# Performance work log

Measured on AMD Instinct MI355X. Metric: run time of the kernel, lower is better.

Reference implementation:

```python
import jax, jax.numpy as jnp
import numpy as np

S, B, H = 1024, 4, 1024
NH, NC = 16, 4            # num_attention_heads, num_combined_heads
HPH = H // NH             # 64
NF = NH // NC             # num_FFN = 4
FFM = 8                   # combined_FFN_multiple
DIN = NC * HPH            # 256, grouped FFN input dim
DHID = FFM * DIN          # 2048, dense_in output dim
DH2 = DHID // 2           # 1024, GLU half / dense_out input dim
EPS = 1e-6
NORM_FACTOR = 1.0 / float(np.sqrt(HPH))


def _ln(x, g, b):
    m = x.mean(-1, keepdims=True)
    v = ((x - m) ** 2).mean(-1, keepdims=True)
    return (x - m) * jax.lax.rsqrt(v + EPS) * g + b


def setup_inputs() -> dict:
    key = jax.random.key(0)
    ks = jax.random.split(key, 10)
    p = lambda k, shape: jax.random.normal(k, shape, jnp.float32) * 0.02
    return {
        "hidden_states": jax.random.normal(ks[0], (S, B, H), jnp.float32),
        "g1": jnp.ones((H,), jnp.float32), "b1": jnp.zeros((H,), jnp.float32),
        "g2": jnp.ones((HPH,), jnp.float32), "b2": jnp.zeros((HPH,), jnp.float32),
        "Wq": p(ks[1], (H, H)), "bq": jnp.zeros((H,), jnp.float32),
        "Wk": p(ks[2], (H, H)), "bk": jnp.zeros((H,), jnp.float32),
        "Wv": p(ks[3], (H, H)), "bv": jnp.zeros((H,), jnp.float32),
        "W_in": p(ks[4], (NF, DIN, DHID)), "b_in": jnp.zeros((NF, DHID), jnp.float32),
        "W_out": p(ks[5], (NF, DH2, DIN)), "b_out": jnp.zeros((NF, DIN), jnp.float32),
        "Wd": p(ks[6], (H, H)), "bd": jnp.zeros((H,), jnp.float32),
    }


def reference(hidden_states, g1, b1, g2, b2, Wq, bq, Wk, bk, Wv, bv,
              W_in, b_in, W_out, b_out, Wd, bd):
    # hidden_states: [S, B, H]
    x = _ln(hidden_states, g1, b1)                       # norm1

    def heads(t):  # [S,B,H] -> [B*NH, S, HPH] (matches view + transpose in torch)
        return jnp.transpose(t.reshape(S, B * NH, HPH), (1, 0, 2))

    q = heads(x @ Wq + bq)
    k = heads(x @ Wk + bk)
    v = heads(x @ Wv + bv)

    # subtraction_gaussian_kernel: pairwise squared euclidean distance
    qk = jnp.einsum('nsd,ntd->nst', q, k)                # [B*NH, S, S]
    q2 = jnp.sum(q * q, axis=-1)
    k2 = jnp.sum(k * k, axis=-1)
    dist = q2[:, :, None] + k2[None if False else slice(None), None, :][0] if False else q2[:, :, None] + k2[:, None, :] - 2.0 * qk
    matmul_result = dist * (-0.5 * NORM_FACTOR)          # scores <= 0

    # Exp sequence op: elementwise exp (softmax replacement, no normalization)
    probs = jnp.exp(matmul_result)

    ctx = jnp.einsum('nst,ntd->nsd', probs, v)           # [B*NH, S, HPH]
    ctx = jnp.transpose(ctx, (1, 0, 2)).reshape(S, B, H)
    ctx = x + ctx                                        # residual with norm1 output (as in source)

    ctx = _ln(ctx.reshape(S, B, NH, HPH), g2, b2)        # per-head norm2

    # grouped FFN over contiguous head subsets (vectorized over the NF groups)
    cg = ctx.reshape(S, B, NF, DIN)
    h = jnp.einsum('sbgi,gio->sbgo', cg, W_in) + b_in    # [S,B,NF,DHID]
    xh, yh = jnp.split(h, 2, axis=-1)
    h = xh * jax.nn.relu(yh)                             # GLU-style x * relu(y)
    og = jnp.einsum('sbgi,gio->sbgo', h, W_out) + b_out  # [S,B,NF,DIN]

    out = og.reshape(S, B, H) @ Wd + bd                  # attention_dense
    return out, matmul_result
```

## Files before the change

kernel.cpp:

```cpp
#include <hip/hip_runtime.h>


typedef __attribute__((ext_vector_type(8))) short short8;
typedef __attribute__((ext_vector_type(4))) float f32x4;

__device__ __forceinline__ unsigned short f2bf(float f) {
  union { float f; unsigned u; } x; x.f = f;
  unsigned r = x.u + 0x7FFFu + ((x.u >> 16) & 1u);
  return (unsigned short)(r >> 16);
}
__device__ __forceinline__ float bf2f(unsigned short u) {
  union { float f; unsigned u; } x; x.u = ((unsigned)u) << 16;
  return x.f;
}
__device__ __forceinline__ void gload16(const unsigned short* g, unsigned short* l) {
  __builtin_amdgcn_global_load_lds(
      (const __attribute__((address_space(1))) unsigned int*)g,
      (__attribute__((address_space(3))) unsigned int*)l, 16, 0, 0);
}

__global__ __launch_bounds__(256) void ln1_kernel(
    const float* __restrict__ x, const float* __restrict__ g,
    const float* __restrict__ b, float* __restrict__ y,
    unsigned short* __restrict__ ybf)
{
  const long base = (long)blockIdx.x * 1024;
  const int c = threadIdx.x * 4;
  float4 v = *(const float4*)(x + base + c);
  float s = v.x + v.y + v.z + v.w;
  float ss = v.x*v.x + v.y*v.y + v.z*v.z + v.w*v.w;
  #pragma unroll
  for (int off = 32; off > 0; off >>= 1) {
    s  += __shfl_xor(s, off);
    ss += __shfl_xor(ss, off);
  }
  __shared__ float sw[4], ssw[4];
  const int wave = threadIdx.x >> 6;
  if ((threadIdx.x & 63) == 0) { sw[wave] = s; ssw[wave] = ss; }
  __syncthreads();
  s  = sw[0] + sw[1] + sw[2] + sw[3];
  ss = ssw[0] + ssw[1] + ssw[2] + ssw[3];
  const float mean = s * (1.0f/1024.0f);
  const float var  = ss * (1.0f/1024.0f) - mean*mean;
  const float rs   = rsqrtf(var + 1e-6f);
  const float4 gv = *(const float4*)(g + c);
  const float4 bv = *(const float4*)(b + c);
  float4 o;
  o.x = (v.x - mean) * rs * gv.x + bv.x;
  o.y = (v.y - mean) * rs * gv.y + bv.y;
  o.z = (v.z - mean) * rs * gv.z + bv.z;
  o.w = (v.w - mean) * rs * gv.w + bv.w;
  *(float4*)(y + base + c) = o;
  ushort4 ob;
  ob.x = f2bf(o.x); ob.y = f2bf(o.y); ob.z = f2bf(o.z); ob.w = f2bf(o.w);
  *(ushort4*)(ybf + base + c) = ob;
}

__global__ __launch_bounds__(256) void transpose_w_kernel(
    const float* __restrict__ W, int K, int N, long wgs,
    unsigned short* __restrict__ WT, long wtgs)
{
  __shared__ float T[32][33];
  const float* Wg = W + (long)blockIdx.z * wgs;
  unsigned short* WTg = WT + (long)blockIdx.z * wtgs;
  const int n0 = blockIdx.x * 32, k0 = blockIdx.y * 32;
  const int t = threadIdx.x;
  const int r = t >> 3, c4 = (t & 7) * 4;
  float4 v = *(const float4*)(Wg + (long)(k0 + r) * N + n0 + c4);
  T[r][c4+0] = v.x; T[r][c4+1] = v.y; T[r][c4+2] = v.z; T[r][c4+3] = v.w;
  __syncthreads();
  ushort4 o;
  o.x = f2bf(T[c4+0][r]); o.y = f2bf(T[c4+1][r]);
  o.z = f2bf(T[c4+2][r]); o.w = f2bf(T[c4+3][r]);
  *(ushort4*)(WTg + (long)(n0 + r) * K + k0 + c4) = o;
}

__global__ __launch_bounds__(256) void transpose_qkvd_kernel(
    const float* __restrict__ Wq, const float* __restrict__ Wk,
    const float* __restrict__ Wv, const float* __restrict__ Wd,
    unsigned short* __restrict__ wqkvT, unsigned short* __restrict__ wdT)
{
  const int z = blockIdx.z;
  const float* W = (z == 0) ? Wq : (z == 1) ? Wk : (z == 2) ? Wv : Wd;
  unsigned short* WT = (z == 3) ? wdT : wqkvT + (long)z * 1048576;
  __shared__ float T[32][33];
  const int n0 = blockIdx.x * 32, k0 = blockIdx.y * 32;
  const int t = threadIdx.x;
  const int r = t >> 3, c4 = (t & 7) * 4;
  float4 v = *(const float4*)(W + (long)(k0 + r) * 1024 + n0 + c4);
  T[r][c4+0] = v.x; T[r][c4+1] = v.y; T[r][c4+2] = v.z; T[r][c4+3] = v.w;
  __syncthreads();
  ushort4 o;
  o.x = f2bf(T[c4+0][r]); o.y = f2bf(T[c4+1][r]);
  o.z = f2bf(T[c4+2][r]); o.w = f2bf(T[c4+3][r]);
  *(ushort4*)(WT + (long)(n0 + r) * 1024 + k0 + c4) = o;
}

__global__ __launch_bounds__(256) void packb_kernel(
    const float* __restrict__ bq, const float* __restrict__ bk,
    const float* __restrict__ bv, float* __restrict__ qb)
{
  const int i = blockIdx.x * 256 + threadIdx.x;
  qb[i] = (i < 1024) ? bq[i] : ((i < 2048) ? bk[i - 1024] : bv[i - 2048]);
}

__global__ __launch_bounds__(256) void mfma_gemm_kernel(
    const unsigned short* __restrict__ A, int lda, long agoff,
    const unsigned short* __restrict__ BT, long bgoff, int K,
    const float* __restrict__ bias, int biasoff,
    unsigned short* __restrict__ Cbf, float* __restrict__ Cf,
    int ldc, int cgoff)
{
  const int g = blockIdx.z;
  const unsigned short* Ag = A + (long)g * agoff;
  const unsigned short* Bg = BT + (long)g * bgoff;
  const float* biasg = bias + (long)g * biasoff;
  const int row0 = blockIdx.y * 128, col0 = blockIdx.x * 128;
  __shared__ __align__(16) unsigned short As[128 * 32];
  __shared__ __align__(16) unsigned short Bs[128 * 32];
  const int tid = threadIdx.x;
  const int w = tid >> 6, l = tid & 63;
  const int ms = (w & 1) << 6, ns = (w >> 1) << 6;
  const int fr = l & 15, fg = l >> 4;
  const int lr = l >> 2;
  const int sslot = (((l & 3) ^ (lr & 3)) << 3);
  const int arow = row0 + (w << 4) + lr;
  const int brow = col0 + (w << 4) + lr;
  const int rsw = fr & 3;
  f32x4 acc[4][4];
  #pragma unroll
  for (int i = 0; i < 4; ++i)
    #pragma unroll
    for (int j = 0; j < 4; ++j) acc[i][j] = (f32x4)0.0f;

  for (int k0 = 0; k0 < K; k0 += 32) {
    gload16(Ag + (long)arow * lda + k0 + sslot,        &As[(w << 4) * 32]);
    gload16(Ag + (long)(arow + 64) * lda + k0 + sslot, &As[(64 + (w << 4)) * 32]);
    gload16(Bg + (long)brow * K + k0 + sslot,          &Bs[(w << 4) * 32]);
    gload16(Bg + (long)(brow + 64) * K + k0 + sslot,   &Bs[(64 + (w << 4)) * 32]);
    __syncthreads();
    short8 af[4], bfr[4];
    #pragma unroll
    for (int i = 0; i < 4; ++i)
      af[i] = *(const short8*)&As[(ms + i*16 + fr) * 32 + ((fg ^ rsw) << 3)];
    #pragma unroll
    for (int j = 0; j < 4; ++j)
      bfr[j] = *(const short8*)&Bs[(ns + j*16 + fr) * 32 + ((fg ^ rsw) << 3)];
    #pragma unroll
    for (int i = 0; i < 4; ++i)
      #pragma unroll
      for (int j = 0; j < 4; ++j)
        acc[i][j] = __builtin_amdgcn_mfma_f32_16x16x32_bf16(af[i], bfr[j], acc[i][j], 0, 0, 0);
    __syncthreads();
  }

  float bj[4];
  #pragma unroll
  for (int j = 0; j < 4; ++j) bj[j] = biasg[col0 + ns + j*16 + fr];
  #pragma unroll
  for (int i = 0; i < 4; ++i)
    #pragma unroll
    for (int r = 0; r < 4; ++r) {
      const long row = row0 + ms + i*16 + (fg << 2) + r;
      const long cbase = row * ldc + (long)g * cgoff + col0 + ns;
      #pragma unroll
      for (int j = 0; j < 4; ++j) {
        const float v = acc[i][j][r] + bj[j];
        if (Cbf) Cbf[cbase + j*16 + fr] = f2bf(v);
        else     __builtin_nontemporal_store(v, &Cf[cbase + j*16 + fr]);
      }
    }
}

__global__ __launch_bounds__(256) void mfma_glu_kernel(
    const unsigned short* __restrict__ A,
    const unsigned short* __restrict__ WT,
    const float* __restrict__ bin,
    unsigned short* __restrict__ H2)
{
  const int g = blockIdx.z;
  const unsigned short* Ag = A + g * 256;
  const unsigned short* Wg = WT + (long)g * 2048 * 256;
  const float* bg = bin + g * 2048;
  const int row0 = blockIdx.y * 128, col0 = blockIdx.x * 64;
  __shared__ __align__(16) unsigned short As[128 * 32];
  __shared__ __align__(16) unsigned short Bxs[64 * 32];
  __shared__ __align__(16) unsigned short Bys[64 * 32];
  const int tid = threadIdx.x;
  const int w = tid >> 6, l = tid & 63;
  const int ms = (w & 1) << 6, ns = (w >> 1) << 5;
  const int fr = l & 15, fg = l >> 4;
  const int lr = l >> 2;
  const int sslot = (((l & 3) ^ (lr & 3)) << 3);
  const int arow = row0 + (w << 4) + lr;
  const int brow = col0 + (w << 4) + lr;
  const int rsw = fr & 3;
  f32x4 ax[4][2], ay[4][2];
  #pragma unroll
  for (int i = 0; i < 4; ++i)
    #pragma unroll
    for (int j = 0; j < 2; ++j) { ax[i][j] = (f32x4)0.0f; ay[i][j] = (f32x4)0.0f; }

  for (int k0 = 0; k0 < 256; k0 += 32) {
    gload16(Ag + (long)arow * 1024 + k0 + sslot,        &As[(w << 4) * 32]);
    gload16(Ag + (long)(arow + 64) * 1024 + k0 + sslot, &As[(64 + (w << 4)) * 32]);
    gload16(Wg + (long)brow * 256 + k0 + sslot,         &Bxs[(w << 4) * 32]);
    gload16(Wg + (long)(1024 + brow) * 256 + k0 + sslot,&Bys[(w << 4) * 32]);
    __syncthreads();
    short8 af[4], bx[2], by[2];
    #pragma unroll
    for (int i = 0; i < 4; ++i)
      af[i] = *(const short8*)&As[(ms + i*16 + fr) * 32 + ((fg ^ rsw) << 3)];
    #pragma unroll
    for (int j = 0; j < 2; ++j) {
      bx[j] = *(const short8*)&Bxs[(ns + j*16 + fr) * 32 + ((fg ^ rsw) << 3)];
      by[j] = *(const short8*)&Bys[(ns + j*16 + fr) * 32 + ((fg ^ rsw) << 3)];
    }
    #pragma unroll
    for (int i = 0; i < 4; ++i)
      #pragma unroll
      for (int j = 0; j < 2; ++j) {
        ax[i][j] = __builtin_amdgcn_mfma_f32_16x16x32_bf16(af[i], bx[j], ax[i][j], 0, 0, 0);
        ay[i][j] = __builtin_amdgcn_mfma_f32_16x16x32_bf16(af[i], by[j], ay[i][j], 0, 0, 0);
      }
    __syncthreads();
  }

  float bxb[2], byb[2];
  #pragma unroll
  for (int j = 0; j < 2; ++j) {
    bxb[j] = bg[col0 + ns + j*16 + fr];
    byb[j] = bg[1024 + col0 + ns + j*16 + fr];
  }
  #pragma unroll
  for (int i = 0; i < 4; ++i)
    #pragma unroll
    for (int r = 0; r < 4; ++r) {
      const long row = row0 + ms + i*16 + (fg << 2) + r;
      #pragma unroll
      for (int j = 0; j < 2; ++j) {
        const float xh = ax[i][j][r] + bxb[j];
        const float yh = ay[i][j][r] + byb[j];
        H2[row * 4096 + g * 1024 + col0 + ns + j*16 + fr] = f2bf(xh * fmaxf(yh, 0.0f));
      }
    }
}

__global__ __launch_bounds__(256) void sumsq_kernel(
    const unsigned short* __restrict__ qkv,
    float* __restrict__ q2g, float* __restrict__ k2g)
{
  const int sb = blockIdx.x;
  const int s = sb >> 2, b = sb & 3;
  const int h = threadIdx.x >> 4, e = threadIdx.x & 15;
  const long base = (long)sb * 3072 + h * 64 + e * 4;
  ushort4 qv = *(const ushort4*)(qkv + base);
  ushort4 kv = *(const ushort4*)(qkv + base + 1024);
  float sq = 0.f, sk = 0.f, f;
  f = bf2f(qv.x); sq = fmaf(f,f,sq); f = bf2f(qv.y); sq = fmaf(f,f,sq);
  f = bf2f(qv.z); sq = fmaf(f,f,sq); f = bf2f(qv.w); sq = fmaf(f,f,sq);
  f = bf2f(kv.x); sk = fmaf(f,f,sk); f = bf2f(kv.y); sk = fmaf(f,f,sk);
  f = bf2f(kv.z); sk = fmaf(f,f,sk); f = bf2f(kv.w); sk = fmaf(f,f,sk);
  #pragma unroll
  for (int off = 1; off < 16; off <<= 1) { sq += __shfl_xor(sq, off); sk += __shfl_xor(sk, off); }
  if (e == 0) {
    q2g[(b * 16 + h) * 1024 + s] = sq;
    k2g[(b * 16 + h) * 1024 + s] = sk;
  }
}

__global__ __launch_bounds__(256) void vtrans_kernel(
    const unsigned short* __restrict__ qkv, unsigned short* __restrict__ vt)
{
  __shared__ unsigned short T[64][72];
  const int n = blockIdx.y, s0 = blockIdx.x * 64;
  const int b = n >> 4, hoff = (n & 15) * 64;
  const int tid = threadIdx.x;
  #pragma unroll
  for (int p = 0; p < 2; ++p) {
    const int r = (tid >> 3) + p * 32, c = (tid & 7) << 3;
    *(short8*)&T[r][c] = *(const short8*)(qkv + ((long)((s0 + r) * 4 + b)) * 3072 + 2048 + hoff + c);
  }
  __syncthreads();
  #pragma unroll
  for (int p = 0; p < 2; ++p) {
    const int d = (tid >> 3) + p * 32, sc = (tid & 7) << 3;
    short8 o;
    #pragma unroll
    for (int j = 0; j < 8; ++j) o[j] = (short)T[sc + j][d];
    *(short8*)(vt + ((long)n * 64 + d) * 1024 + s0 + sc) = o;
  }
}

__global__ __launch_bounds__(256) void attn_kernel(
    const unsigned short* __restrict__ qkv, const unsigned short* __restrict__ vt,
    const float* __restrict__ q2g, const float* __restrict__ k2g,
    float* __restrict__ ctx, float* __restrict__ scores)
{
  const int n = blockIdx.y;
  const int s0 = blockIdx.x * 64;
  const int b = n >> 4, hoff = (n & 15) * 64;
  __shared__ __align__(16) unsigned short Qs[64][72];
  __shared__ __align__(16) unsigned short Ks[64 * 64];
  __shared__ __align__(16) unsigned short VTl[64 * 64];
  __shared__ __align__(16) unsigned short Ps[64][72];
  __shared__ float q2s[64];
  const int tid = threadIdx.x, w = tid >> 6, l = tid & 63;
  const int fr = l & 15, fg = l >> 4;
  const int lr8 = l >> 3, ls8 = l & 7;
  const int sslot = ((ls8 ^ lr8) << 3);
  const int rsw = fr & 7;

  #pragma unroll
  for (int p = 0; p < 2; ++p) {
    const int r = (tid >> 3) + p * 32, c = (tid & 7) << 3;
    *(short8*)&Qs[r][c] = *(const short8*)(qkv + ((long)((s0 + r) * 4 + b)) * 3072 + hoff + c);
  }
  if (tid < 64) q2s[tid] = q2g[n * 1024 + s0 + tid];

  f32x4 o[4];
  #pragma unroll
  for (int i = 0; i < 4; ++i) o[i] = (f32x4)0.0f;

  for (int t0 = 0; t0 < 1024; t0 += 64) {
    #pragma unroll
    for (int p = 0; p < 2; ++p) {
      const int rowb = p * 32 + w * 8;
      gload16(qkv + ((long)((t0 + rowb + lr8) * 4 + b)) * 3072 + 1024 + hoff + sslot,
              &Ks[rowb * 64]);
      gload16(vt + ((long)n * 64 + rowb + lr8) * 1024 + t0 + sslot,
              &VTl[rowb * 64]);
    }
    const float k2v = k2g[n * 1024 + t0 + (w << 4) + fr];
    __syncthreads();

    f32x4 c4[4];
    #pragma unroll
    for (int i = 0; i < 4; ++i) c4[i] = (f32x4)0.0f;
    #pragma unroll
    for (int ks = 0; ks < 2; ++ks) {
      const short8 bfr = *(const short8*)&Ks[((w << 4) + fr) * 64 + ((((ks << 2) + fg) ^ rsw) << 3)];
      #pragma unroll
      for (int i = 0; i < 4; ++i) {
        const short8 af = *(const short8*)&Qs[i*16 + fr][(ks << 5) + (fg << 3)];
        c4[i] = __builtin_amdgcn_mfma_f32_16x16x32_bf16(af, bfr, c4[i], 0, 0, 0);
      }
    }
    #pragma unroll
    for (int i = 0; i < 4; ++i)
      #pragma unroll
      for (int r4 = 0; r4 < 4; ++r4) {
        const int srow = i*16 + (fg << 2) + r4;
        const float m = (2.0f * c4[i][r4] - q2s[srow] - k2v) * 0.0625f;
        __builtin_nontemporal_store(m,
            &scores[(long)n * 1048576 + (long)(s0 + srow) * 1024 + t0 + (w << 4) + fr]);
        Ps[srow][(w << 4) + fr] = f2bf(__expf(m));
      }
    __syncthreads();

    #pragma unroll
    for (int ks = 0; ks < 2; ++ks) {
      const short8 vb = *(const short8*)&VTl[((w << 4) + fr) * 64 + ((((ks << 2) + fg) ^ rsw) << 3)];
      #pragma unroll
      for (int i = 0; i < 4; ++i) {
        const short8 pa = *(const short8*)&Ps[i*16 + fr][(ks << 5) + (fg << 3)];
        o[i] = __builtin_amdgcn_mfma_f32_16x16x32_bf16(pa, vb, o[i], 0, 0, 0);
      }
    }
    __syncthreads();
  }

  #pragma unroll
  for (int i = 0; i < 4; ++i)
    #pragma unroll
    for (int r4 = 0; r4 < 4; ++r4) {
      const int srow = s0 + i*16 + (fg << 2) + r4;
      ctx[((long)(srow * 4 + b)) * 1024 + hoff + (w << 4) + fr] = o[i][r4];
    }
}

__global__ __launch_bounds__(256) void ln2res_kernel(
    const float* __restrict__ xln, const float* __restrict__ ctx,
    const float* __restrict__ g2, const float* __restrict__ b2,
    unsigned short* __restrict__ ctx2)
{
  const int lane = threadIdx.x & 63;
  const long row = (long)blockIdx.x * 4 + (threadIdx.x >> 6);
  const long idx = row * 64 + lane;
  const float v = xln[idx] + ctx[idx];
  float s = v, ss = v * v;
  #pragma unroll
  for (int off = 32; off > 0; off >>= 1) {
    s  += __shfl_xor(s, off);
    ss += __shfl_xor(ss, off);
  }
  const float mean = s * (1.0f/64.0f);
  const float var  = ss * (1.0f/64.0f) - mean*mean;
  const float rs   = rsqrtf(var + 1e-6f);
  ctx2[idx] = f2bf((v - mean) * rs * g2[lane] + b2[lane]);
}

extern "C" void kernel_launch(void* const* d_in, const int* in_sizes, int n_in,
                              void* d_out, int out_size, void* d_ws, size_t ws_size,
                              hipStream_t stream) {
  const float* hs   = (const float*)d_in[0];
  const float* g1   = (const float*)d_in[1];
  const float* b1   = (const float*)d_in[2];
  const float* g2   = (const float*)d_in[3];
  const float* b2   = (const float*)d_in[4];
  const float* Wq   = (const float*)d_in[5];
  const float* bq   = (const float*)d_in[6];
  const float* Wk   = (const float*)d_in[7];
  const float* bk   = (const float*)d_in[8];
  const float* Wv   = (const float*)d_in[9];
  const float* bv   = (const float*)d_in[10];
  const float* Win  = (const float*)d_in[11];
  const float* bin  = (const float*)d_in[12];
  const float* Wout = (const float*)d_in[13];
  const float* bout = (const float*)d_in[14];
  const float* Wd   = (const float*)d_in[15];
  const float* bd   = (const float*)d_in[16];

  char* ws = (char*)d_ws;
  float*          xln   = (float*)(ws + 0);
  unsigned short* xbf   = (unsigned short*)(ws + 16777216);
  unsigned short* qkv   = (unsigned short*)(ws + 25165824);
  float*          ctx   = (float*)(ws + 50331648);
  unsigned short* ctx2  = (unsigned short*)(ws + 67108864);
  unsigned short* wqkvT = (unsigned short*)(ws + 75497472);
  unsigned short* winT  = (unsigned short*)(ws + 81788928);
  unsigned short* woutT = (unsigned short*)(ws + 85983232);
  unsigned short* wdT   = (unsigned short*)(ws + 88080384);
  float*          qkvb  = (float*)(ws + 90177536);
  unsigned short* vt    = (unsigned short*)(ws + 90189824);
  float*          q2g   = (float*)(ws + 98578432);
  float*          k2g   = (float*)(ws + 98840576);
  unsigned short* h2    = (unsigned short*)(ws + 16777216);
  unsigned short* og    = (unsigned short*)(ws + 0);

  float* out0 = (float*)d_out;
  float* out1 = out0 + 4194304;

  ln1_kernel<<<4096, 256, 0, stream>>>(hs, g1, b1, xln, xbf);

  transpose_qkvd_kernel<<<dim3(32,32,4), 256, 0, stream>>>(Wq, Wk, Wv, Wd, wqkvT, wdT);
  transpose_w_kernel<<<dim3(64,8,4), 256, 0, stream>>>(Win, 256, 2048, 524288, winT, 524288);
  transpose_w_kernel<<<dim3(8,32,4), 256, 0, stream>>>(Wout, 1024, 256, 262144, woutT, 262144);
  packb_kernel<<<12, 256, 0, stream>>>(bq, bk, bv, qkvb);

  mfma_gemm_kernel<<<dim3(24,32,1), 256, 0, stream>>>(
      xbf, 1024, 0, wqkvT, 0, 1024, qkvb, 0, qkv, nullptr, 3072, 0);

  sumsq_kernel<<<4096, 256, 0, stream>>>(qkv, q2g, k2g);
  vtrans_kernel<<<dim3(16,64), 256, 0, stream>>>(qkv, vt);

  attn_kernel<<<dim3(16,64), 256, 0, stream>>>(qkv, vt, q2g, k2g, ctx, out1);

  ln2res_kernel<<<16384, 256, 0, stream>>>(xln, ctx, g2, b2, ctx2);

  mfma_glu_kernel<<<dim3(16,32,4), 256, 0, stream>>>(ctx2, winT, bin, h2);

  mfma_gemm_kernel<<<dim3(2,32,4), 256, 0, stream>>>(
      h2, 4096, 1024, woutT, 262144, 1024, bout, 256, og, nullptr, 1024, 256);

  mfma_gemm_kernel<<<dim3(8,32,1), 256, 0, stream>>>(
      og, 1024, 0, wdT, 0, 1024, bd, 0, nullptr, out0, 1024, 0);
}
```

Before: 268.3 us.

## Double-buffer GEMM/attention tiles, swap MFMA operands for vector stores, fuse prep kernels

Adds LDS double buffering to the generic GEMM, the GLU GEMM and the attention kernel, so the next K/V or A/B tile is prefetched while the current one is computed. This drops one barrier per iteration. MFMA operands are swapped so each lane holds four consecutive output columns, which allows vectorized float4 and packed-bf16 stores (v_cvt_pk_bf16_f32) for the scores, ctx, H2 and GEMM outputs. The sumsq and V-transpose kernels are fused into one prep kernel, and the score scale is folded into an fma. LDS use doubles, which may reduce occupancy.

```diff
diff --git a/kernel.cpp b/kernel.cpp
--- a/kernel.cpp
+++ b/kernel.cpp
@@ -12,6 +12,11 @@
 __device__ __forceinline__ float bf2f(unsigned short u) {
   union { float f; unsigned u; } x; x.u = ((unsigned)u) << 16;
   return x.f;
+}
+__device__ __forceinline__ unsigned cvtpk(float a, float b) {
+  unsigned r;
+  asm("v_cvt_pk_bf16_f32 %0, %1, %2" : "=v"(r) : "v"(a), "v"(b));
+  return r;
 }
 __device__ __forceinline__ void gload16(const unsigned short* g, unsigned short* l) {
   __builtin_amdgcn_global_load_lds(
@@ -116,8 +121,8 @@
   const unsigned short* Bg = BT + (long)g * bgoff;
   const float* biasg = bias + (long)g * biasoff;
   const int row0 = blockIdx.y * 128, col0 = blockIdx.x * 128;
-  __shared__ __align__(16) unsigned short As[128 * 32];
-  __shared__ __align__(16) unsigned short Bs[128 * 32];
+  __shared__ __align__(16) unsigned short As[2][128 * 32];
+  __shared__ __align__(16) unsigned short Bs[2][128 * 32];
   const int tid = threadIdx.x;
   const int w = tid >> 6, l = tid & 63;
   const int ms = (w & 1) << 6, ns = (w >> 1) << 6;
@@ -133,43 +138,55 @@
     #pragma unroll
     for (int j = 0; j < 4; ++j) acc[i][j] = (f32x4)0.0f;
 
-  for (int k0 = 0; k0 < K; k0 += 32) {
-    gload16(Ag + (long)arow * lda + k0 + sslot,        &As[(w << 4) * 32]);
-    gload16(Ag + (long)(arow + 64) * lda + k0 + sslot, &As[(64 + (w << 4)) * 32]);
-    gload16(Bg + (long)brow * K + k0 + sslot,          &Bs[(w << 4) * 32]);
-    gload16(Bg + (long)(brow + 64) * K + k0 + sslot,   &Bs[(64 + (w << 4)) * 32]);
+  const int nt = K >> 5;
+  gload16(Ag + (long)arow * lda + sslot,        &As[0][(w << 4) * 32]);
+  gload16(Ag + (long)(arow + 64) * lda + sslot, &As[0][(64 + (w << 4)) * 32]);
+  gload16(Bg + (long)brow * K + sslot,          &Bs[0][(w << 4) * 32]);
+  gload16(Bg + (long)(brow + 64) * K + sslot,   &Bs[0][(64 + (w << 4)) * 32]);
+  __syncthreads();
+  int cur = 0;
+  for (int t = 0; t < nt; ++t) {
+    if (t + 1 < nt) {
+      const int k0 = (t + 1) << 5;
+      gload16(Ag + (long)arow * lda + k0 + sslot,        &As[cur ^ 1][(w << 4) * 32]);
+      gload16(Ag + (long)(arow + 64) * lda + k0 + sslot, &As[cur ^ 1][(64 + (w << 4)) * 32]);
+      gload16(Bg + (long)brow * K + k0 + sslot,          &Bs[cur ^ 1][(w << 4) * 32]);
+      gload16(Bg + (long)(brow + 64) * K + k0 + sslot,   &Bs[cur ^ 1][(64 + (w << 4)) * 32]);
+    }
+    short8 af[4], bfr[4];
+    #pragma unroll
+    for (int i = 0; i < 4; ++i)
+      af[i] = *(const short8*)&As[cur][(ms + i*16 + fr) * 32 + ((fg ^ rsw) << 3)];
+    #pragma unroll
+    for (int j = 0; j < 4; ++j)
+      bfr[j] = *(const short8*)&Bs[cur][(ns + j*16 + fr) * 32 + ((fg ^ rsw) << 3)];
+    #pragma unroll
+    for (int i = 0; i < 4; ++i)
+      #pragma unroll
+      for (int j = 0; j < 4; ++j)
+        acc[i][j] = __builtin_amdgcn_mfma_f32_16x16x32_bf16(bfr[j], af[i], acc[i][j], 0, 0, 0);
     __syncthreads();
-    short8 af[4], bfr[4];
-    #pragma unroll
-    for (int i = 0; i < 4; ++i)
-      af[i] = *(const short8*)&As[(ms + i*16 + fr) * 32 + ((fg ^ rsw) << 3)];
-    #pragma unroll
-    for (int j = 0; j < 4; ++j)
-      bfr[j] = *(const short8*)&Bs[(ns + j*16 + fr) * 32 + ((fg ^ rsw) << 3)];
-    #pragma unroll
-    for (int i = 0; i < 4; ++i)
-      #pragma unroll
-      for (int j = 0; j < 4; ++j)
-        acc[i][j] = __builtin_amdgcn_mfma_f32_16x16x32_bf16(af[i], bfr[j], acc[i][j], 0, 0, 0);
-    __syncthreads();
-  }
-
-  float bj[4];
-  #pragma unroll
-  for (int j = 0; j < 4; ++j) bj[j] = biasg[col0 + ns + j*16 + fr];
-  #pragma unroll
-  for (int i = 0; i < 4; ++i)
-    #pragma unroll
-    for (int r = 0; r < 4; ++r) {
-      const long row = row0 + ms + i*16 + (fg << 2) + r;
-      const long cbase = row * ldc + (long)g * cgoff + col0 + ns;
-      #pragma unroll
-      for (int j = 0; j < 4; ++j) {
-        const float v = acc[i][j][r] + bj[j];
-        if (Cbf) Cbf[cbase + j*16 + fr] = f2bf(v);
-        else     __builtin_nontemporal_store(v, &Cf[cbase + j*16 + fr]);
-      }
-    }
+    cur ^= 1;
+  }
+
+  #pragma unroll
+  for (int j = 0; j < 4; ++j) {
+    const float4 bj4 = *(const float4*)(biasg + col0 + ns + j*16 + (fg << 2));
+    #pragma unroll
+    for (int i = 0; i < 4; ++i) {
+      const long row = row0 + ms + i*16 + fr;
+      const long cb = row * ldc + (long)g * cgoff + col0 + ns + j*16 + (fg << 2);
+      const float v0 = acc[i][j][0] + bj4.x, v1 = acc[i][j][1] + bj4.y;
+      const float v2 = acc[i][j][2] + bj4.z, v3 = acc[i][j][3] + bj4.w;
+      if (Cbf) {
+        uint2 pk; pk.x = cvtpk(v0, v1); pk.y = cvtpk(v2, v3);
+        *(uint2*)(Cbf + cb) = pk;
+      } else {
+        f32x4 o = {v0, v1, v2, v3};
+        __builtin_nontemporal_store(o, (f32x4*)(Cf + cb));
+      }
+    }
+  }
 }
 
 __global__ __launch_bounds__(256) void mfma_glu_kernel(
@@ -183,9 +200,9 @@
   const unsigned short* Wg = WT + (long)g * 2048 * 256;
   const float* bg = bin + g * 2048;
   const int row0 = blockIdx.y * 128, col0 = blockIdx.x * 64;
-  __shared__ __align__(16) unsigned short As[128 * 32];
-  __shared__ __align__(16) unsigned short Bxs[64 * 32];
-  __shared__ __align__(16) unsigned short Bys[64 * 32];
+  __shared__ __align__(16) unsigned short As[2][128 * 32];
+  __shared__ __align__(16) unsigned short Bxs[2][64 * 32];
+  __shared__ __align__(16) unsigned short Bys[2][64 * 32];
   const int tid = threadIdx.x;
   const int w = tid >> 6, l = tid & 63;
   const int ms = (w & 1) << 6, ns = (w >> 1) << 5;
@@ -201,85 +218,96 @@
     #pragma unroll
     for (int j = 0; j < 2; ++j) { ax[i][j] = (f32x4)0.0f; ay[i][j] = (f32x4)0.0f; }
 
-  for (int k0 = 0; k0 < 256; k0 += 32) {
-    gload16(Ag + (long)arow * 1024 + k0 + sslot,        &As[(w << 4) * 32]);
-    gload16(Ag + (long)(arow + 64) * 1024 + k0 + sslot, &As[(64 + (w << 4)) * 32]);
-    gload16(Wg + (long)brow * 256 + k0 + sslot,         &Bxs[(w << 4) * 32]);
-    gload16(Wg + (long)(1024 + brow) * 256 + k0 + sslot,&Bys[(w << 4) * 32]);
+  gload16(Ag + (long)arow * 1024 + sslot,         &As[0][(w << 4) * 32]);
+  gload16(Ag + (long)(arow + 64) * 1024 + sslot,  &As[0][(64 + (w << 4)) * 32]);
+  gload16(Wg + (long)brow * 256 + sslot,          &Bxs[0][(w << 4) * 32]);
+  gload16(Wg + (long)(1024 + brow) * 256 + sslot, &Bys[0][(w << 4) * 32]);
+  __syncthreads();
+  int cur = 0;
+  for (int t = 0; t < 8; ++t) {
+    if (t + 1 < 8) {
+      const int k0 = (t + 1) << 5;
+      gload16(Ag + (long)arow * 1024 + k0 + sslot,         &As[cur ^ 1][(w << 4) * 32]);
+      gload16(Ag + (long)(arow + 64) * 1024 + k0 + sslot,  &As[cur ^ 1][(64 + (w << 4)) * 32]);
+      gload16(Wg + (long)brow * 256 + k0 + sslot,          &Bxs[cur ^ 1][(w << 4) * 32]);
+      gload16(Wg + (long)(1024 + brow) * 256 + k0 + sslot, &Bys[cur ^ 1][(w << 4) * 32]);
+    }
+    short8 af[4], bx[2], by[2];
+    #pragma unroll
+    for (int i = 0; i < 4; ++i)
+      af[i] = *(const short8*)&As[cur][(ms + i*16 + fr) * 32 + ((fg ^ rsw) << 3)];
+    #pragma unroll
+    for (int j = 0; j < 2; ++j) {
+      bx[j] = *(const short8*)&Bxs[cur][(ns + j*16 + fr) * 32 + ((fg ^ rsw) << 3)];
+      by[j] = *(const short8*)&Bys[cur][(ns + j*16 + fr) * 32 + ((fg ^ rsw) << 3)];
+    }
+    #pragma unroll
+    for (int i = 0; i < 4; ++i)
+      #pragma unroll
+      for (int j = 0; j < 2; ++j) {
+        ax[i][j] = __builtin_amdgcn_mfma_f32_16x16x32_bf16(bx[j], af[i], ax[i][j], 0, 0, 0);
+        ay[i][j] = __builtin_amdgcn_mfma_f32_16x16x32_bf16(by[j], af[i], ay[i][j], 0, 0, 0);
+      }
     __syncthreads();
-    short8 af[4], bx[2], by[2];
-    #pragma unroll
-    for (int i = 0; i < 4; ++i)
-      af[i] = *(const short8*)&As[(ms + i*16 + fr) * 32 + ((fg ^ rsw) << 3)];
-    #pragma unroll
-    for (int j = 0; j < 2; ++j) {
-      bx[j] = *(const short8*)&Bxs[(ns + j*16 + fr) * 32 + ((fg ^ rsw) << 3)];
-      by[j] = *(const short8*)&Bys[(ns + j*16 + fr) * 32 + ((fg ^ rsw) << 3)];
-    }
-    #pragma unroll
-    for (int i = 0; i < 4; ++i)
-      #pragma unroll
-      for (int j = 0; j < 2; ++j) {
-        ax[i][j] = __builtin_amdgcn_mfma_f32_16x16x32_bf16(af[i], bx[j], ax[i][j], 0, 0, 0);
-        ay[i][j] = __builtin_amdgcn_mfma_f32_16x16x32_bf16(af[i], by[j], ay[i][j], 0, 0, 0);
-      }
-    __syncthreads();
-  }
-
-  float bxb[2], byb[2];
+    cur ^= 1;
+  }
+
   #pragma unroll
   for (int j = 0; j < 2; ++j) {
-    bxb[j] = bg[col0 + ns + j*16 + fr];
-    byb[j] = bg[1024 + col0 + ns + j*16 + fr];
-  }
-  #pragma unroll
-  for (int i = 0; i < 4; ++i)
-    #pragma unroll
-    for (int r = 0; r < 4; ++r) {
-      const long row = row0 + ms + i*16 + (fg << 2) + r;
-      #pragma unroll
-      for (int j = 0; j < 2; ++j) {
-        const float xh = ax[i][j][r] + bxb[j];
-        const float yh = ay[i][j][r] + byb[j];
-        H2[row * 4096 + g * 1024 + col0 + ns + j*16 + fr] = f2bf(xh * fmaxf(yh, 0.0f));
-      }
-    }
-}
-
-__global__ __launch_bounds__(256) void sumsq_kernel(
+    const float4 bx4 = *(const float4*)(bg + col0 + ns + j*16 + (fg << 2));
+    const float4 by4 = *(const float4*)(bg + 1024 + col0 + ns + j*16 + (fg << 2));
+    #pragma unroll
+    for (int i = 0; i < 4; ++i) {
+      const long row = row0 + ms + i*16 + fr;
+      const long cb = row * 4096 + g * 1024 + col0 + ns + j*16 + (fg << 2);
+      float o4[4];
+      const float* bxp = &bx4.x; const float* byp = &by4.x;
+      #pragma unroll
+      for (int r4 = 0; r4 < 4; ++r4) {
+        const float xh = ax[i][j][r4] + bxp[r4];
+        const float yh = ay[i][j][r4] + byp[r4];
+        o4[r4] = xh * fmaxf(yh, 0.0f);
+      }
+      uint2 pk; pk.x = cvtpk(o4[0], o4[1]); pk.y = cvtpk(o4[2], o4[3]);
+      *(uint2*)(H2 + cb) = pk;
+    }
+  }
+}
+
+__global__ __launch_bounds__(256) void prep_attn_kernel(
     const unsigned short* __restrict__ qkv,
-    float* __restrict__ q2g, float* __restrict__ k2g)
-{
-  const int sb = blockIdx.x;
-  const int s = sb >> 2, b = sb & 3;
-  const int h = threadIdx.x >> 4, e = threadIdx.x & 15;
-  const long base = (long)sb * 3072 + h * 64 + e * 4;
-  ushort4 qv = *(const ushort4*)(qkv + base);
-  ushort4 kv = *(const ushort4*)(qkv + base + 1024);
-  float sq = 0.f, sk = 0.f, f;
-  f = bf2f(qv.x); sq = fmaf(f,f,sq); f = bf2f(qv.y); sq = fmaf(f,f,sq);
-  f = bf2f(qv.z); sq = fmaf(f,f,sq); f = bf2f(qv.w); sq = fmaf(f,f,sq);
-  f = bf2f(kv.x); sk = fmaf(f,f,sk); f = bf2f(kv.y); sk = fmaf(f,f,sk);
-  f = bf2f(kv.z); sk = fmaf(f,f,sk); f = bf2f(kv.w); sk = fmaf(f,f,sk);
-  #pragma unroll
-  for (int off = 1; off < 16; off <<= 1) { sq += __shfl_xor(sq, off); sk += __shfl_xor(sk, off); }
-  if (e == 0) {
-    q2g[(b * 16 + h) * 1024 + s] = sq;
-    k2g[(b * 16 + h) * 1024 + s] = sk;
-  }
-}
-
-__global__ __launch_bounds__(256) void vtrans_kernel(
-    const unsigned short* __restrict__ qkv, unsigned short* __restrict__ vt)
-{
-  __shared__ unsigned short T[64][72];
+    float* __restrict__ q2g, float* __restrict__ k2g,
+    unsigned short* __restrict__ vt)
+{
   const int n = blockIdx.y, s0 = blockIdx.x * 64;
   const int b = n >> 4, hoff = (n & 15) * 64;
   const int tid = threadIdx.x;
+  __shared__ unsigned short T[64][72];
   #pragma unroll
   for (int p = 0; p < 2; ++p) {
     const int r = (tid >> 3) + p * 32, c = (tid & 7) << 3;
     *(short8*)&T[r][c] = *(const short8*)(qkv + ((long)((s0 + r) * 4 + b)) * 3072 + 2048 + hoff + c);
+  }
+  {
+    const int r = tid >> 2, e = tid & 3;
+    const long base = ((long)((s0 + r) * 4 + b)) * 3072 + hoff + (e << 4);
+    float sq = 0.f, sk = 0.f;
+    #pragma unroll
+    for (int ch = 0; ch < 2; ++ch) {
+      short8 q8 = *(const short8*)(qkv + base + (ch << 3));
+      short8 k8 = *(const short8*)(qkv + base + 1024 + (ch << 3));
+      #pragma unroll
+      for (int ee = 0; ee < 8; ++ee) {
+        float f = bf2f((unsigned short)q8[ee]); sq = fmaf(f, f, sq);
+        f = bf2f((unsigned short)k8[ee]); sk = fmaf(f, f, sk);
+      }
+    }
+    sq += __shfl_xor(sq, 1); sq += __shfl_xor(sq, 2);
+    sk += __shfl_xor(sk, 1); sk += __shfl_xor(sk, 2);
+    if (e == 0) {
+      q2g[n * 1024 + s0 + r] = sq;
+      k2g[n * 1024 + s0 + r] = sk;
+    }
   }
   __syncthreads();
   #pragma unroll
@@ -301,10 +329,9 @@
   const int s0 = blockIdx.x * 64;
   const int b = n >> 4, hoff = (n & 15) * 64;
   __shared__ __align__(16) unsigned short Qs[64][72];
-  __shared__ __align__(16) unsigned short Ks[64 * 64];
-  __shared__ __align__(16) unsigned short VTl[64 * 64];
+  __shared__ __align__(16) unsigned short Ks[2][64 * 64];
+  __shared__ __align__(16) unsigned short VTl[2][64 * 64];
   __shared__ __align__(16) unsigned short Ps[64][72];
-  __shared__ float q2s[64];
   const int tid = threadIdx.x, w = tid >> 6, l = tid & 63;
   const int fr = l & 15, fg = l >> 4;
   const int lr8 = l >> 3, ls8 = l & 7;
@@ -316,67 +343,84 @@
     const int r = (tid >> 3) + p * 32, c = (tid & 7) << 3;
     *(short8*)&Qs[r][c] = *(const short8*)(qkv + ((long)((s0 + r) * 4 + b)) * 3072 + hoff + c);
   }
-  if (tid < 64) q2s[tid] = q2g[n * 1024 + s0 + tid];
+  float q2m[4];
+  #pragma unroll
+  for (int i = 0; i < 4; ++i) q2m[i] = -0.0625f * q2g[n * 1024 + s0 + i*16 + fr];
+
+  #pragma unroll
+  for (int p = 0; p < 2; ++p) {
+    const int rowb = p * 32 + w * 8;
+    gload16(qkv + ((long)((rowb + lr8) * 4 + b)) * 3072 + 1024 + hoff + sslot, &Ks[0][rowb * 64]);
+    gload16(vt + ((long)n * 64 + rowb + lr8) * 1024 + sslot,                   &VTl[0][rowb * 64]);
+  }
+  __syncthreads();
 
   f32x4 o[4];
   #pragma unroll
   for (int i = 0; i < 4; ++i) o[i] = (f32x4)0.0f;
 
+  int cur = 0;
   for (int t0 = 0; t0 < 1024; t0 += 64) {
-    #pragma unroll
-    for (int p = 0; p < 2; ++p) {
-      const int rowb = p * 32 + w * 8;
-      gload16(qkv + ((long)((t0 + rowb + lr8) * 4 + b)) * 3072 + 1024 + hoff + sslot,
-              &Ks[rowb * 64]);
-      gload16(vt + ((long)n * 64 + rowb + lr8) * 1024 + t0 + sslot,
-              &VTl[rowb * 64]);
-    }
-    const float k2v = k2g[n * 1024 + t0 + (w << 4) + fr];
+    if (t0 + 64 < 1024) {
+      #pragma unroll
+      for (int p = 0; p < 2; ++p) {
+        const int rowb = p * 32 + w * 8;
+        gload16(qkv + ((long)((t0 + 64 + rowb + lr8) * 4 + b)) * 3072 + 1024 + hoff + sslot,
+                &Ks[cur ^ 1][rowb * 64]);
+        gload16(vt + ((long)n * 64 + rowb + lr8) * 1024 + t0 + 64 + sslot,
+                &VTl[cur ^ 1][rowb * 64]);
+      }
+    }
+    const float4 k2v4 = *(const float4*)(k2g + n * 1024 + t0 + (w << 4) + (fg << 2));
+    const float k2m[4] = {-0.0625f*k2v4.x, -0.0625f*k2v4.y, -0.0625f*k2v4.z, -0.0625f*k2v4.w};
+
+    f32x4 c4[4];
+    #pragma unroll
+    for (int i = 0; i < 4; ++i) c4[i] = (f32x4)0.0f;
+    #pragma unroll
+    for (int ks = 0; ks < 2; ++ks) {
+      const short8 kf = *(const short8*)&Ks[cur][((w << 4) + fr) * 64 + ((((ks << 2) + fg) ^ rsw) << 3)];
+      #pragma unroll
+      for (int i = 0; i < 4; ++i) {
+        const short8 qf = *(const short8*)&Qs[i*16 + fr][(ks << 5) + (fg << 3)];
+        c4[i] = __builtin_amdgcn_mfma_f32_16x16x32_bf16(kf, qf, c4[i], 0, 0, 0);
+      }
+    }
+    #pragma unroll
+    for (int i = 0; i < 4; ++i) {
+      f32x4 sc;
+      float pe[4];
+      #pragma unroll
+      for (int r4 = 0; r4 < 4; ++r4) {
+        const float m = fmaf(c4[i][r4], 0.125f, q2m[i] + k2m[r4]);
+        sc[r4] = m;
+        pe[r4] = __expf(m);
+      }
+      __builtin_nontemporal_store(sc,
+          (f32x4*)(scores + (long)n * 1048576 + (long)(s0 + i*16 + fr) * 1024 + t0 + (w << 4) + (fg << 2)));
+      uint2 pk; pk.x = cvtpk(pe[0], pe[1]); pk.y = cvtpk(pe[2], pe[3]);
+      *(uint2*)&Ps[i*16 + fr][(w << 4) + (fg << 2)] = pk;
+    }
     __syncthreads();
 
-    f32x4 c4[4];
-    #pragma unroll
-    for (int i = 0; i < 4; ++i) c4[i] = (f32x4)0.0f;
     #pragma unroll
     for (int ks = 0; ks < 2; ++ks) {
-      const short8 bfr = *(const short8*)&Ks[((w << 4) + fr) * 64 + ((((ks << 2) + fg) ^ rsw) << 3)];
+      const short8 vb = *(const short8*)&VTl[cur][((w << 4) + fr) * 64 + ((((ks << 2) + fg) ^ rsw) << 3)];
       #pragma unroll
       for (int i = 0; i < 4; ++i) {
-        const short8 af = *(const short8*)&Qs[i*16 + fr][(ks << 5) + (fg << 3)];
-        c4[i] = __builtin_amdgcn_mfma_f32_16x16x32_bf16(af, bfr, c4[i], 0, 0, 0);
-      }
-    }
-    #pragma unroll
-    for (int i = 0; i < 4; ++i)
-      #pragma unroll
-      for (int r4 = 0; r4 < 4; ++r4) {
-        const int srow = i*16 + (fg << 2) + r4;
-        const float m = (2.0f * c4[i][r4] - q2s[srow] - k2v) * 0.0625f;
-        __builtin_nontemporal_store(m,
-            &scores[(long)n * 1048576 + (long)(s0 + srow) * 1024 + t0 + (w << 4) + fr]);
-        Ps[srow][(w << 4) + fr] = f2bf(__expf(m));
-      }
+        const short8 pf = *(const short8*)&Ps[i*16 + fr][(ks << 5) + (fg << 3)];
+        o[i] = __builtin_amdgcn_mfma_f32_16x16x32_bf16(vb, pf, o[i], 0, 0, 0);
+      }
+    }
     __syncthreads();
-
-    #pragma unroll
-    for (int ks = 0; ks < 2; ++ks) {
-      const short8 vb = *(const short8*)&VTl[((w << 4) + fr) * 64 + ((((ks << 2) + fg) ^ rsw) << 3)];
-      #pragma unroll
-      for (int i = 0; i < 4; ++i) {
-        const short8 pa = *(const short8*)&Ps[i*16 + fr][(ks << 5) + (fg << 3)];
-        o[i] = __builtin_amdgcn_mfma_f32_16x16x32_bf16(pa, vb, o[i], 0, 0, 0);
-      }
-    }
-    __syncthreads();
-  }
-
-  #pragma unroll
-  for (int i = 0; i < 4; ++i)
-    #pragma unroll
-    for (int r4 = 0; r4 < 4; ++r4) {
-      const int srow = s0 + i*16 + (fg << 2) + r4;
-      ctx[((long)(srow * 4 + b)) * 1024 + hoff + (w << 4) + fr] = o[i][r4];
-    }
+    cur ^= 1;
+  }
+
+  #pragma unroll
+  for (int i = 0; i < 4; ++i) {
+    const float4 ov = make_float4(o[i][0], o[i][1], o[i][2], o[i][3]);
+    *(float4*)(ctx + ((long)((s0 + i*16 + fr) * 4 + b)) * 1024 + hoff + (w << 4) + (fg << 2)) = ov;
+  }
 }
 
 __global__ __launch_bounds__(256) void ln2res_kernel(
@@ -451,8 +495,7 @@
   mfma_gemm_kernel<<<dim3(24,32,1), 256, 0, stream>>>(
       xbf, 1024, 0, wqkvT, 0, 1024, qkvb, 0, qkv, nullptr, 3072, 0);
 
-  sumsq_kernel<<<4096, 256, 0, stream>>>(qkv, q2g, k2g);
-  vtrans_kernel<<<dim3(16,64), 256, 0, stream>>>(qkv, vt);
+  prep_attn_kernel<<<dim3(16,64), 256, 0, stream>>>(qkv, q2g, k2g, vt);
 
   attn_kernel<<<dim3(16,64), 256, 0, stream>>>(qkv, vt, q2g, k2g, ctx, out1);
 
```

Result: no change. 272.4 us (+1.5%).
